# Performance work log

Hardware: AMD Instinct MI355X
Metric: run time of the kernel (lower is better)

## Reference

```python
import jax, jax.numpy as jnp
import numpy as np

NBITS = 2
Q_T = 1
Q_ALPHA = 0.9
NORM_PPF_0_75 = 0.6745
IN_FEATURES = 4096
OUT_FEATURES = 4096
TOKENS = 8192

# signed bit encodings: rows of {-1,+1}^NBITS for codes 0..2^NBITS-1
_bitvecs = np.unpackbits(np.arange(2 ** NBITS, dtype=np.uint8).reshape(-1, 1), axis=1)[:, -NBITS:]
ENCODINGS = jnp.asarray(_bitvecs.astype(np.float32) * 2.0 - 1.0)  # [2^nbits, nbits]


def setup_inputs() -> dict:
    key = jax.random.key(0)
    k1, k2, k3 = jax.random.split(key, 3)
    m, n = IN_FEATURES, OUT_FEATURES
    x = jax.random.normal(k1, (TOKENS, m), dtype=jnp.float32)
    # matches linear.weight.data.normal_(0, sqrt(2/(m+n)))
    weight = jax.random.normal(k2, (n, m), dtype=jnp.float32) * np.sqrt(2.0 / (m + n))
    bias = jax.random.normal(k3, (n,), dtype=jnp.float32) * 0.01
    base = NORM_PPF_0_75 * (2.0 / n) ** 0.5 / 2 ** (NBITS - 1)
    basis = jnp.asarray([base * 2.0 ** i for i in range(NBITS)], dtype=jnp.float32)
    return {"x": x, "weight": weight, "bias": bias, "basis": basis}


def _quantize(w, basis, encodings):
    # qlevels[k] = <encodings[k], basis>, then sort levels ascending
    qlevels = encodings @ basis                      # [2^nbits]
    order = jnp.argsort(qlevels)
    qlevels = qlevels[order]
    enc = encodings[order]                           # [2^nbits, nbits]
    # midpoints between adjacent levels; bucketize replaces the per-level mask loop:
    # level i iff  thres[i-1] < w <= thres[i]  (w <= thres[0] -> 0, w > thres[-1] -> last)
    thres = 0.5 * (qlevels[:-1] + qlevels[1:])       # [2^nbits - 1]
    idx = jnp.searchsorted(thres, w.ravel(), side="left")  # [N]
    wq = qlevels[idx].reshape(w.shape)               # quantized weights
    wb = enc[idx]                                    # [N, nbits] signed codes
    return wq, wb


def reference(x, weight, bias, basis):
    # training-mode learned quantization: quantize, then least-squares basis refit
    v = basis
    w_flat = weight.ravel()
    for _ in range(Q_T):
        wq, wb = _quantize(weight, v, ENCODINGS)
        # solve (wb^T wb) v = wb^T w   (nbits x nbits system)
        v = jnp.linalg.solve(wb.T @ wb, wb.T @ w_flat)
    new_basis = Q_ALPHA * basis + (1.0 - Q_ALPHA) * v
    # straight-through estimator: forward uses wq, backward passes grad to weight
    wq_ste = weight + jax.lax.stop_gradient(wq - weight)
    out = x @ wq_ste.T + bias                        # [tokens, out_features]
    del new_basis  # buffer update; not part of the forward output tensor
    return out
```

## Files before the change

kernel.cpp:

```cpp
#include <hip/hip_runtime.h>
#include <hip/hip_bf16.h>


#define M_TOK 8192
#define N_OUT 4096
#define K_IN  4096

typedef __attribute__((ext_vector_type(8))) short short8;
typedef __attribute__((ext_vector_type(4))) float floatx4;

typedef __attribute__((address_space(1))) const void gvoid_t;
typedef __attribute__((address_space(3))) void lvoid_t;

__device__ __forceinline__ ushort f2bf(float f) {
    unsigned u = __float_as_uint(f);
    u += 0x7fffu + ((u >> 16) & 1u);
    return (ushort)(u >> 16);
}

#define PREP_XBLK 2048
#define PREP_WBLK 1024

__global__ __launch_bounds__(256) void prep(
        const float4* __restrict__ x,  short8* __restrict__ xb,
        const float4* __restrict__ w,  const float* __restrict__ basis,
        short8* __restrict__ wqo) {
    if (blockIdx.x < PREP_XBLK) {
        const int tid    = blockIdx.x * 256 + threadIdx.x;
        const int stride = PREP_XBLK * 256;
        const int n8     = (M_TOK * K_IN) / 8;
        for (int i = tid; i < n8; i += stride) {
            float4 a = x[2 * i], b = x[2 * i + 1];
            short8 o;
            o[0] = (short)f2bf(a.x); o[1] = (short)f2bf(a.y);
            o[2] = (short)f2bf(a.z); o[3] = (short)f2bf(a.w);
            o[4] = (short)f2bf(b.x); o[5] = (short)f2bf(b.y);
            o[6] = (short)f2bf(b.z); o[7] = (short)f2bf(b.w);
            xb[i] = o;
        }
    } else {
        float b0 = basis[0], b1 = basis[1];
        float l0 = -b0 - b1, l1 = -b0 + b1, l2 = b0 - b1, l3 = b0 + b1;
        float t;
        if (l0 > l1) { t = l0; l0 = l1; l1 = t; }
        if (l2 > l3) { t = l2; l2 = l3; l3 = t; }
        if (l0 > l2) { t = l0; l0 = l2; l2 = t; }
        if (l1 > l3) { t = l1; l1 = l3; l3 = t; }
        if (l1 > l2) { t = l1; l1 = l2; l2 = t; }
        const float t0 = 0.5f * (l0 + l1), t1 = 0.5f * (l1 + l2), t2 = 0.5f * (l2 + l3);
        const int tid    = (blockIdx.x - PREP_XBLK) * 256 + threadIdx.x;
        const int stride = PREP_WBLK * 256;
        const int n8     = (N_OUT * K_IN) / 8;
#define QF(vv) ((vv > t1) ? ((vv > t2) ? l3 : l2) : ((vv > t0) ? l1 : l0))
        for (int i = tid; i < n8; i += stride) {
            float4 a = w[2 * i], b = w[2 * i + 1];
            short8 o;
            o[0] = (short)f2bf(QF(a.x)); o[1] = (short)f2bf(QF(a.y));
            o[2] = (short)f2bf(QF(a.z)); o[3] = (short)f2bf(QF(a.w));
            o[4] = (short)f2bf(QF(b.x)); o[5] = (short)f2bf(QF(b.y));
            o[6] = (short)f2bf(QF(b.z)); o[7] = (short)f2bf(QF(b.w));
            wqo[i] = o;
        }
#undef QF
    }
}

__global__ __launch_bounds__(256) void gemm_bt(
        const ushort* __restrict__ A,
        const ushort* __restrict__ B,
        const float* __restrict__ bias,
        float* __restrict__ C) {
    __shared__ ushort As[128 * 64];
    __shared__ ushort Bs[128 * 64];

    const int lane = threadIdx.x & 63;
    const int wv   = threadIdx.x >> 6;
    const int bm0  = blockIdx.y * 128;
    const int bn0  = blockIdx.x * 128;
    const int wm   = (wv >> 1) * 64;
    const int wn   = (wv & 1) * 64;

    floatx4 acc[4][4] = {};

    const int lr = lane >> 3;
    const int lc = lane & 7;
    const ushort* ag = A + (size_t)(bm0 + wv * 32 + lr) * K_IN + (lc ^ lr) * 8;
    const ushort* bg = B + (size_t)(bn0 + wv * 32 + lr) * K_IN + (lc ^ lr) * 8;
    ushort* asl = As + (wv * 32) * 64;
    ushort* bsl = Bs + (wv * 32) * 64;

    const int mrow = lane & 15;
    const int quad = lane >> 4;
    const int cswz = (quad ^ (mrow & 7)) * 8;

    for (int kt = 0; kt < K_IN / 64; ++kt) {
#pragma unroll
        for (int t = 0; t < 4; ++t) {
            __builtin_amdgcn_global_load_lds((gvoid_t*)(ag + (size_t)t * 8 * K_IN),
                                             (lvoid_t*)(asl + t * 8 * 64), 16, 0, 0);
            __builtin_amdgcn_global_load_lds((gvoid_t*)(bg + (size_t)t * 8 * K_IN),
                                             (lvoid_t*)(bsl + t * 8 * 64), 16, 0, 0);
        }
        ag += 64; bg += 64;
        __syncthreads();
#pragma unroll
        for (int ks = 0; ks < 2; ++ks) {
            short8 af[4], bfv[4];
#pragma unroll
            for (int i = 0; i < 4; ++i)
                af[i] = *(const short8*)(As + (wm + i * 16 + mrow) * 64 + (cswz ^ (ks * 32)));
#pragma unroll
            for (int j = 0; j < 4; ++j)
                bfv[j] = *(const short8*)(Bs + (wn + j * 16 + mrow) * 64 + (cswz ^ (ks * 32)));
#pragma unroll
            for (int i = 0; i < 4; ++i)
#pragma unroll
                for (int j = 0; j < 4; ++j)
                    acc[i][j] = __builtin_amdgcn_mfma_f32_16x16x32_bf16(
                        af[i], bfv[j], acc[i][j], 0, 0, 0);
        }
        __syncthreads();
    }

    const int r0 = (lane >> 4) * 4;
    const int cc = lane & 15;
#pragma unroll
    for (int j = 0; j < 4; ++j) {
        const int col = bn0 + wn + j * 16 + cc;
        const float bj = bias[col];
#pragma unroll
        for (int i = 0; i < 4; ++i) {
#pragma unroll
            for (int r = 0; r < 4; ++r) {
                const int row = bm0 + wm + i * 16 + r0 + r;
                C[(size_t)row * N_OUT + col] = acc[i][j][r] + bj;
            }
        }
    }
}

extern "C" void kernel_launch(void* const* d_in, const int* in_sizes, int n_in,
                              void* d_out, int out_size, void* d_ws, size_t ws_size,
                              hipStream_t stream) {
    const float* x     = (const float*)d_in[0];
    const float* w     = (const float*)d_in[1];
    const float* bias  = (const float*)d_in[2];
    const float* basis = (const float*)d_in[3];
    float* out = (float*)d_out;

    ushort* Xb = (ushort*)d_ws;
    ushort* Wq = Xb + (size_t)M_TOK * K_IN;

    prep<<<PREP_XBLK + PREP_WBLK, 256, 0, stream>>>(
        (const float4*)x, (short8*)Xb, (const float4*)w, basis, (short8*)Wq);

    {
        dim3 grid(N_OUT / 128, M_TOK / 128);
        gemm_bt<<<grid, 256, 0, stream>>>(Xb, Wq, bias, out);
    }
}
```

Baseline: 590.2 us.

## Rewrite GEMM as 256x256 double-buffered pipelined kernel with interleaved loads and MFMA

Replaces the 128x128 single-buffered GEMM with a 256x256-tile, 512-thread kernel. It uses 128KB of double-buffered dynamic LDS and splits each K-step into four barrier-separated phases, so global-to-LDS prefetch of the next tile is interleaved with MFMA work under raised scheduling priority. It also remaps block IDs for L2 locality and drops the per-iteration full syncs. Each thread now holds more accumulators and the kernel needs 128KB of LDS per block, which raises register pressure and limits occupancy.

```diff
diff --git a/kernel.cpp b/kernel.cpp
--- a/kernel.cpp
+++ b/kernel.cpp
@@ -65,75 +65,144 @@
     }
 }
 
-__global__ __launch_bounds__(256) void gemm_bt(
+
+#define NIT 32
+
+#define BAR() do { asm volatile("" ::: "memory"); \
+                   __builtin_amdgcn_s_barrier(); \
+                   asm volatile("" ::: "memory"); \
+                   __builtin_amdgcn_sched_barrier(0); } while (0)
+#define VMC6() asm volatile("s_waitcnt vmcnt(6)" ::: "memory")
+#define VMC0() asm volatile("s_waitcnt vmcnt(0)" ::: "memory")
+
+#define STAGE_A(tt, h) do { const int _p = (tt) & 1;                          \
+    __builtin_amdgcn_global_load_lds(                                         \
+        (gvoid_t*)(ag + (size_t)((h) * 128) * K_IN + (tt) * 64),              \
+        (lvoid_t*)(As + _p * 16384 + ((h) * 128 + wid * 16) * 64), 16, 0, 0); \
+    __builtin_amdgcn_global_load_lds(                                         \
+        (gvoid_t*)(ag + (size_t)((h) * 128 + 8) * K_IN + (tt) * 64),          \
+        (lvoid_t*)(As + _p * 16384 + ((h) * 128 + wid * 16 + 8) * 64), 16, 0, 0); \
+} while (0)
+#define STAGE_B(tt, h) do { const int _p = (tt) & 1;                          \
+    __builtin_amdgcn_global_load_lds(                                         \
+        (gvoid_t*)(bg + (size_t)((h) * 128) * K_IN + (tt) * 64),              \
+        (lvoid_t*)(Bs + _p * 16384 + ((h) * 128 + wid * 16) * 64), 16, 0, 0); \
+    __builtin_amdgcn_global_load_lds(                                         \
+        (gvoid_t*)(bg + (size_t)((h) * 128 + 8) * K_IN + (tt) * 64),          \
+        (lvoid_t*)(Bs + _p * 16384 + ((h) * 128 + wid * 16 + 8) * 64), 16, 0, 0); \
+} while (0)
+
+#define MFMA_PAIR(MA, MB) do {                                                \
+    __builtin_amdgcn_s_setprio(1);                                           \
+    _Pragma("unroll") for (int nj = 0; nj < 4; ++nj) {                        \
+        acc[MA][nj] = __builtin_amdgcn_mfma_f32_16x16x32_bf16(                \
+            af[MA][0], bfv[nj][0], acc[MA][nj], 0, 0, 0);                     \
+        acc[MA][nj] = __builtin_amdgcn_mfma_f32_16x16x32_bf16(                \
+            af[MA][1], bfv[nj][1], acc[MA][nj], 0, 0, 0);                     \
+    }                                                                         \
+    _Pragma("unroll") for (int nj = 0; nj < 4; ++nj) {                        \
+        acc[MB][nj] = __builtin_amdgcn_mfma_f32_16x16x32_bf16(                \
+            af[MB][0], bfv[nj][0], acc[MB][nj], 0, 0, 0);                     \
+        acc[MB][nj] = __builtin_amdgcn_mfma_f32_16x16x32_bf16(                \
+            af[MB][1], bfv[nj][1], acc[MB][nj], 0, 0, 0);                     \
+    }                                                                         \
+    __builtin_amdgcn_s_setprio(0);                                            \
+} while (0)
+
+#define GROUP4(PB, TS1, C1, TS2, CM) do {                                     \
+    const ushort* Ab = As + (PB) * 16384;                                     \
+    const ushort* Bb = Bs + (PB) * 16384;                                     \
+    short8 af[8][2], bfv[4][2];                                               \
+                            \
+    _Pragma("unroll") for (int nj = 0; nj < 4; ++nj)                          \
+        _Pragma("unroll") for (int ks = 0; ks < 2; ++ks)                      \
+            bfv[nj][ks] = *(const short8*)(Bb + (wn + nj * 16 + mrow) * 64 + (cswz ^ (ks * 32))); \
+    _Pragma("unroll") for (int mi = 0; mi < 2; ++mi)                          \
+        _Pragma("unroll") for (int ks = 0; ks < 2; ++ks)                      \
+            af[mi][ks] = *(const short8*)(Ab + (wm + mi * 16 + mrow) * 64 + (cswz ^ (ks * 32))); \
+    if (C1) { STAGE_A(TS1, 1); }                                              \
+    BAR();                                                                    \
+    MFMA_PAIR(0, 1);                                                          \
+    BAR();                                                                    \
+                                    \
+    _Pragma("unroll") for (int mi = 2; mi < 6; ++mi)                          \
+        _Pragma("unroll") for (int ks = 0; ks < 2; ++ks)                      \
+            af[mi][ks] = *(const short8*)(Ab + (wm + mi * 16 + mrow) * 64 + (cswz ^ (ks * 32))); \
+    if (CM) { STAGE_B(TS2, 0); }                                              \
+    BAR();                                                                    \
+    MFMA_PAIR(2, 3);                                                          \
+    BAR();                                                                    \
+                                   \
+    _Pragma("unroll") for (int mi = 6; mi < 8; ++mi)                          \
+        _Pragma("unroll") for (int ks = 0; ks < 2; ++ks)                      \
+            af[mi][ks] = *(const short8*)(Ab + (wm + mi * 16 + mrow) * 64 + (cswz ^ (ks * 32))); \
+    if (CM) { STAGE_B(TS2, 1); }                                              \
+    BAR();                                                                    \
+    MFMA_PAIR(4, 5);                                                          \
+    BAR();                                                                    \
+                                                       \
+    if (CM) { STAGE_A(TS2, 0); VMC6(); } else { VMC0(); }                     \
+    BAR();                                                                    \
+    MFMA_PAIR(6, 7);                                                          \
+    BAR();                                                                    \
+} while (0)
+
+extern "C" __global__ __launch_bounds__(512, 2) void gemm256(
         const ushort* __restrict__ A,
         const ushort* __restrict__ B,
         const float* __restrict__ bias,
         float* __restrict__ C) {
-    __shared__ ushort As[128 * 64];
-    __shared__ ushort Bs[128 * 64];
-
-    const int lane = threadIdx.x & 63;
-    const int wv   = threadIdx.x >> 6;
-    const int bm0  = blockIdx.y * 128;
-    const int bn0  = blockIdx.x * 128;
-    const int wm   = (wv >> 1) * 64;
-    const int wn   = (wv & 1) * 64;
-
-    floatx4 acc[4][4] = {};
-
-    const int lr = lane >> 3;
-    const int lc = lane & 7;
-    const ushort* ag = A + (size_t)(bm0 + wv * 32 + lr) * K_IN + (lc ^ lr) * 8;
-    const ushort* bg = B + (size_t)(bn0 + wv * 32 + lr) * K_IN + (lc ^ lr) * 8;
-    ushort* asl = As + (wv * 32) * 64;
-    ushort* bsl = Bs + (wv * 32) * 64;
+    extern __shared__ ushort smem[];
+    ushort* As = smem;
+    ushort* Bs = smem + 32768;
+
+    const int tid  = threadIdx.x;
+    const int lane = tid & 63;
+    const int wid  = tid >> 6;
+    const int wr   = wid >> 2;
+    const int wc   = wid & 3;
+    const int wm   = wr * 128;
+    const int wn   = wc * 64;
+
+    const int bid = blockIdx.x;
+    const int swz = (bid & 7) * 64 + (bid >> 3);
+    const int bn0 = (swz & 15) * 256;
+    const int bm0 = (swz >> 4) * 256;
+
+    const int lr = lane >> 3, lc = lane & 7;
+    const ushort* ag = A + (size_t)(bm0 + wid * 16 + lr) * K_IN + (lc ^ lr) * 8;
+    const ushort* bg = B + (size_t)(bn0 + wid * 16 + lr) * K_IN + (lc ^ lr) * 8;
 
     const int mrow = lane & 15;
     const int quad = lane >> 4;
     const int cswz = (quad ^ (mrow & 7)) * 8;
 
-    for (int kt = 0; kt < K_IN / 64; ++kt) {
-#pragma unroll
-        for (int t = 0; t < 4; ++t) {
-            __builtin_amdgcn_global_load_lds((gvoid_t*)(ag + (size_t)t * 8 * K_IN),
-                                             (lvoid_t*)(asl + t * 8 * 64), 16, 0, 0);
-            __builtin_amdgcn_global_load_lds((gvoid_t*)(bg + (size_t)t * 8 * K_IN),
-                                             (lvoid_t*)(bsl + t * 8 * 64), 16, 0, 0);
-        }
-        ag += 64; bg += 64;
-        __syncthreads();
-#pragma unroll
-        for (int ks = 0; ks < 2; ++ks) {
-            short8 af[4], bfv[4];
-#pragma unroll
-            for (int i = 0; i < 4; ++i)
-                af[i] = *(const short8*)(As + (wm + i * 16 + mrow) * 64 + (cswz ^ (ks * 32)));
-#pragma unroll
-            for (int j = 0; j < 4; ++j)
-                bfv[j] = *(const short8*)(Bs + (wn + j * 16 + mrow) * 64 + (cswz ^ (ks * 32)));
-#pragma unroll
-            for (int i = 0; i < 4; ++i)
-#pragma unroll
-                for (int j = 0; j < 4; ++j)
-                    acc[i][j] = __builtin_amdgcn_mfma_f32_16x16x32_bf16(
-                        af[i], bfv[j], acc[i][j], 0, 0, 0);
-        }
-        __syncthreads();
+    floatx4 acc[8][4] = {};
+
+    STAGE_B(0, 0); STAGE_B(0, 1); STAGE_A(0, 0); STAGE_A(0, 1);
+    STAGE_B(1, 0); STAGE_B(1, 1); STAGE_A(1, 0);
+    VMC6();
+    BAR();
+
+#pragma unroll 1
+    for (int it = 0; it < NIT; ++it) {
+        const bool more = (it + 1 < NIT);
+        GROUP4(0, 2 * it + 1, true, 2 * it + 2, more);
+        GROUP4(1, 2 * it + 2, more, 2 * it + 3, more);
     }
 
     const int r0 = (lane >> 4) * 4;
     const int cc = lane & 15;
 #pragma unroll
-    for (int j = 0; j < 4; ++j) {
-        const int col = bn0 + wn + j * 16 + cc;
+    for (int nj = 0; nj < 4; ++nj) {
+        const int col = bn0 + wn + nj * 16 + cc;
         const float bj = bias[col];
 #pragma unroll
-        for (int i = 0; i < 4; ++i) {
+        for (int mi = 0; mi < 8; ++mi) {
 #pragma unroll
             for (int r = 0; r < 4; ++r) {
-                const int row = bm0 + wm + i * 16 + r0 + r;
-                C[(size_t)row * N_OUT + col] = acc[i][j][r] + bj;
+                const int row = bm0 + wm + mi * 16 + r0 + r;
+                C[(size_t)row * N_OUT + col] = acc[mi][nj][r] + bj;
             }
         }
     }
@@ -154,8 +223,7 @@
     prep<<<PREP_XBLK + PREP_WBLK, 256, 0, stream>>>(
         (const float4*)x, (short8*)Xb, (const float4*)w, basis, (short8*)Wq);
 
-    {
-        dim3 grid(N_OUT / 128, M_TOK / 128);
-        gemm_bt<<<grid, 256, 0, stream>>>(Xb, Wq, bias, out);
-    }
-}
+    (void)hipFuncSetAttribute((const void*)gemm256,
+                              hipFuncAttributeMaxDynamicSharedMemorySize, 131072);
+    gemm256<<<dim3(512), 512, 131072, stream>>>(Xb, Wq, bias, out);
+}
```

New measurement: 490.2 us. -16.9%, faster.
